# Optimization experiments

Hardware: AMD Instinct MI355X
Metric: run time of the kernel (lower is better)

The kernel has to match this reference:

```python
import jax, jax.numpy as jnp
import numpy as np

N_A, N_P, E = 50000, 50000, 600000
H, D = 8, 16
C = H * D  # hidden_channels = 128
OUT = 16
F_A, F_P = 256, 128
NEG_SLOPE = 0.2
EPS = 1e-5


def setup_inputs():
    key = jax.random.key(0)
    ks = jax.random.split(key, 16)
    return {
        'x_author': jax.random.normal(ks[0], (N_A, F_A), jnp.float32),
        'x_paper': jax.random.normal(ks[1], (N_P, F_P), jnp.float32),
        'W_a': jax.random.normal(ks[2], (F_A, C), jnp.float32) / np.sqrt(F_A).astype(np.float32),
        'b_a': jnp.zeros((C,), jnp.float32),
        'W_p': jax.random.normal(ks[3], (F_P, C), jnp.float32) / np.sqrt(F_P).astype(np.float32),
        'b_p': jnp.zeros((C,), jnp.float32),
        'att_src_ap': jax.random.normal(ks[4], (H, D), jnp.float32) * 0.1,
        'att_dst_ap': jax.random.normal(ks[5], (H, D), jnp.float32) * 0.1,
        'att_src_pp': jax.random.normal(ks[6], (H, D), jnp.float32) * 0.1,
        'att_dst_pp': jax.random.normal(ks[7], (H, D), jnp.float32) * 0.1,
        'k_W': jax.random.normal(ks[8], (C, C), jnp.float32) / np.sqrt(C).astype(np.float32),
        'k_b': jnp.zeros((C,), jnp.float32),
        'q': jax.random.normal(ks[9], (C,), jnp.float32) * 0.1,
        'norm_w': jnp.ones((C,), jnp.float32),
        'norm_b': jnp.zeros((C,), jnp.float32),
        'norm_ms': jnp.ones((C,), jnp.float32),
        'lin_W': jax.random.normal(ks[10], (C, OUT), jnp.float32) / np.sqrt(C).astype(np.float32),
        'lin_b': jnp.zeros((OUT,), jnp.float32),
        'edge_ap': jax.random.randint(ks[11], (2, E), 0, N_A),
        'edge_pp': jax.random.randint(ks[12], (2, E), 0, N_P),
    }


def _edge_type_out(h_src, h_dst, edge, a_src, a_dst, n_dst):
    # Node-level attention for one edge type (PyG HANConv per-metapath GAT).
    alpha_s = jnp.einsum('nhd,hd->nh', h_src, a_src)  # [N_src, H]
    alpha_d = jnp.einsum('nhd,hd->nh', h_dst, a_dst)  # [N_dst, H]
    src, dst = edge[0], edge[1]
    alpha = alpha_s[src] + alpha_d[dst]                       # [E, H]
    alpha = jnp.where(alpha >= 0, alpha, NEG_SLOPE * alpha)   # leaky_relu(0.2)
    m = jax.ops.segment_max(alpha, dst, num_segments=n_dst)
    e = jnp.exp(alpha - m[dst])
    denom = jax.ops.segment_sum(e, dst, num_segments=n_dst)
    attn = e / denom[dst]                                     # softmax over incoming edges
    msg = h_src[src] * attn[:, :, None]                       # [E, H, D]
    out = jax.ops.segment_sum(msg, dst, num_segments=n_dst)   # [n_dst, H, D]
    return jax.nn.relu(out.reshape(n_dst, H * D))


def reference(x_author, x_paper, W_a, b_a, W_p, b_p, att_src_ap, att_dst_ap,
              att_src_pp, att_dst_pp, k_W, k_b, q, norm_w, norm_b, norm_ms,
              lin_W, lin_b, edge_ap, edge_pp):
    # per-node-type projections -> [N, H, D]
    h_a = (x_author @ W_a + b_a).reshape(N_A, H, D)
    h_p = (x_paper @ W_p + b_p).reshape(N_P, H, D)
    # per-edge-type node-level attention + aggregation (both target 'paper')
    out_ap = _edge_type_out(h_a, h_p, edge_ap, att_src_ap, att_dst_ap, N_P)
    out_pp = _edge_type_out(h_p, h_p, edge_pp, att_src_pp, att_dst_pp, N_P)
    # semantic-level attention across the R=2 meta-paths
    outs = jnp.stack([out_ap, out_pp], axis=0)               # [R, N_P, C]
    w = jnp.tanh(outs @ k_W + k_b).mean(axis=1) @ q          # [R]
    beta = jax.nn.softmax(w)
    out = jnp.einsum('rnc,r->nc', outs, beta)                # [N_P, C]
    # GraphNorm (single graph: stats over all nodes)
    mean = out.mean(axis=0)
    o = out - mean * norm_ms
    var = (o * o).mean(axis=0)
    o = norm_w * o / jnp.sqrt(var + EPS) + norm_b
    # final classifier
    return o @ lin_W + lin_b
```

## Files before the change

kernel.cpp:

```cpp
#include <hip/hip_runtime.h>
#include <math.h>

#define NN   50000
#define EE   600000
#define CCH  128
#define HH   8
#define DD   16
#define OUTC 16
#define NEG  0.2f
#define EPSN 1e-5f
#define SLICE_DIV 12500

typedef _Float16 f16x8 __attribute__((ext_vector_type(8)));
typedef float    f32x4 __attribute__((ext_vector_type(4)));

__device__ __forceinline__ float fast_tanh(float x) {
    x = fminf(10.f, fmaxf(-10.f, x));
    float e = __expf(2.f * x);
    return (e - 1.f) / (e + 1.f);
}

__global__ __launch_bounds__(256) void prep_k(const float* __restrict__ W_a,
        const float* __restrict__ W_p, const float* __restrict__ k_W,
        const float* __restrict__ lin_W, const int* __restrict__ ea,
        const int* __restrict__ ep, _Float16* __restrict__ Wt_a,
        _Float16* __restrict__ Wt_p, _Float16* __restrict__ kWt,
        _Float16* __restrict__ linWt, int* __restrict__ counts)
{
    int b = blockIdx.x;
    if (b < 264) {
        int id = b * 256 + threadIdx.x;
        if (id < 32768) {
            int k = id >> 7, n = id & 127;
            Wt_a[n * 256 + k] = (_Float16)W_a[id];
        } else if (id < 49152) {
            int i = id - 32768; int k = i >> 7, n = i & 127;
            Wt_p[n * 128 + k] = (_Float16)W_p[i];
        } else if (id < 65536) {
            int i = id - 49152; int k = i >> 7, n = i & 127;
            kWt[n * 128 + k] = (_Float16)k_W[i];
        } else if (id < 67584) {
            int i = id - 65536; int k = i >> 4, n = i & 15;
            linWt[n * 128 + k] = (_Float16)lin_W[i];
        }
    } else {
        int bb = b - 264;
        int slice = bb & 7;
        int chunk = bb >> 3;
        int lo = slice * SLICE_DIV, hi = lo + SLICE_DIV;
        int base = chunk * 1024;
#pragma unroll
        for (int it = 0; it < 4; ++it) {
            int e = base + it * 256 + threadIdx.x;
            if (e < EE) {
                int d = ea[EE + e];
                if (d >= lo && d < hi) atomicAdd(&counts[d], 1);
            } else if (e < 2 * EE) {
                int d = NN + ep[e];
                if (d >= lo && d < hi) atomicAdd(&counts[d], 1);
            }
        }
    }
}

__global__ __launch_bounds__(256) void gemm2_k(const float* __restrict__ X_a,
        const float* __restrict__ X_p, const _Float16* __restrict__ Wt_a,
        const _Float16* __restrict__ Wt_p, const float* __restrict__ b_a,
        const float* __restrict__ b_p,
        const float* __restrict__ att_s_ap, const float* __restrict__ att_d_ap,
        const float* __restrict__ att_s_pp, const float* __restrict__ att_d_pp,
        _Float16* __restrict__ h_a, _Float16* __restrict__ h_p,
        float* __restrict__ as_ap, float* __restrict__ ad_ap,
        float* __restrict__ as_pp, float* __restrict__ ad_pp, int GBn)
{
    __shared__ _Float16 As[64][40];
    __shared__ _Float16 Bs[128][40];
    const int which = ((int)blockIdx.x >= GBn) ? 1 : 0;
    const float* X = which ? X_p : X_a;
    const _Float16* Wt = which ? Wt_p : Wt_a;
    const float* bias = which ? b_p : b_a;
    _Float16* Y = which ? h_p : h_a;
    const int K = which ? 128 : 256;
    const int t = threadIdx.x;
    const int r0 = (blockIdx.x - which * GBn) * 64;
    const int lane = t & 63;
    const int wv = t >> 6;
    const int m16 = lane & 15;
    const int kq = lane >> 4;
    f32x4 acc[8];
#pragma unroll
    for (int i = 0; i < 8; ++i) acc[i] = (f32x4){0.f, 0.f, 0.f, 0.f};

    const int ar = t >> 2;
    const int ak = (t & 3) * 8;
    const int br = t >> 1;
    const int bk = (t & 1) * 16;

    for (int kc = 0; kc < K; kc += 32) {
        int row = r0 + ar;
        f16x8 av;
        if (row < NN) {
            const float4* gp = (const float4*)&X[row * K + kc + ak];
            float4 x0 = gp[0], x1 = gp[1];
            av[0] = (_Float16)x0.x; av[1] = (_Float16)x0.y;
            av[2] = (_Float16)x0.z; av[3] = (_Float16)x0.w;
            av[4] = (_Float16)x1.x; av[5] = (_Float16)x1.y;
            av[6] = (_Float16)x1.z; av[7] = (_Float16)x1.w;
        } else {
#pragma unroll
            for (int j = 0; j < 8; ++j) av[j] = (_Float16)0.f;
        }
        *(f16x8*)&As[ar][ak] = av;
        const f16x8* wp = (const f16x8*)&Wt[br * K + kc + bk];
        *(f16x8*)&Bs[br][bk]     = wp[0];
        *(f16x8*)&Bs[br][bk + 8] = wp[1];
        __syncthreads();
        f16x8 af = *(const f16x8*)&As[wv * 16 + m16][kq * 8];
#pragma unroll
        for (int i = 0; i < 8; ++i) {
            f16x8 bf = *(const f16x8*)&Bs[i * 16 + m16][kq * 8];
            acc[i] = __builtin_amdgcn_mfma_f32_16x16x32_f16(af, bf, acc[i], 0, 0, 0);
        }
        __syncthreads();
    }
    const int rbase = r0 + wv * 16 + kq * 4;
#pragma unroll
    for (int i = 0; i < 8; ++i) {
        int col = i * 16 + m16;
        float b = bias[col];
        float hv[4];
#pragma unroll
        for (int rr = 0; rr < 4; ++rr) hv[rr] = acc[i][rr] + b;
#pragma unroll
        for (int rr = 0; rr < 4; ++rr)
            if (rbase + rr < NN) Y[(rbase + rr) * 128 + col] = (_Float16)hv[rr];
        if (which == 0) {
            float av = att_s_ap[i * 16 + m16];
            float p[4];
#pragma unroll
            for (int rr = 0; rr < 4; ++rr) p[rr] = hv[rr] * av;
#pragma unroll
            for (int x = 1; x < 16; x <<= 1)
#pragma unroll
                for (int rr = 0; rr < 4; ++rr) p[rr] += __shfl_xor(p[rr], x, 64);
            if (m16 == 0) {
#pragma unroll
                for (int rr = 0; rr < 4; ++rr)
                    if (rbase + rr < NN) as_ap[(rbase + rr) * 8 + i] = p[rr];
            }
        } else {
            float a1 = att_d_ap[i * 16 + m16];
            float a2 = att_s_pp[i * 16 + m16];
            float a3 = att_d_pp[i * 16 + m16];
            float p1[4], p2[4], p3[4];
#pragma unroll
            for (int rr = 0; rr < 4; ++rr) {
                p1[rr] = hv[rr] * a1; p2[rr] = hv[rr] * a2; p3[rr] = hv[rr] * a3;
            }
#pragma unroll
            for (int x = 1; x < 16; x <<= 1) {
#pragma unroll
                for (int rr = 0; rr < 4; ++rr) {
                    p1[rr] += __shfl_xor(p1[rr], x, 64);
                    p2[rr] += __shfl_xor(p2[rr], x, 64);
                    p3[rr] += __shfl_xor(p3[rr], x, 64);
                }
            }
            if (m16 == 0) {
#pragma unroll
                for (int rr = 0; rr < 4; ++rr) {
                    if (rbase + rr < NN) {
                        ad_ap[(rbase + rr) * 8 + i] = p1[rr];
                        as_pp[(rbase + rr) * 8 + i] = p2[rr];
                        ad_pp[(rbase + rr) * 8 + i] = p3[rr];
                    }
                }
            }
        }
    }
}

__global__ __launch_bounds__(256) void scan1_k(const int* __restrict__ counts,
        int* __restrict__ incl, int* __restrict__ bsum) {
    __shared__ int s[256];
    int t = threadIdx.x;
    int i = blockIdx.x * 256 + t;
    int v = (i < 2 * NN) ? counts[i] : 0;
    s[t] = v; __syncthreads();
    for (int off = 1; off < 256; off <<= 1) {
        int x = (t >= off) ? s[t - off] : 0;
        __syncthreads();
        s[t] += x;
        __syncthreads();
    }
    incl[i] = s[t];
    if (t == 255) bsum[blockIdx.x] = s[255];
}

__global__ __launch_bounds__(512) void scan2_k(int* __restrict__ bsum, int nb) {
    __shared__ int s[512];
    int t = threadIdx.x;
    int v = (t < nb) ? bsum[t] : 0;
    s[t] = v; __syncthreads();
    for (int off = 1; off < 512; off <<= 1) {
        int x = (t >= off) ? s[t - off] : 0;
        __syncthreads();
        s[t] += x;
        __syncthreads();
    }
    if (t < nb) bsum[t] = s[t] - v;
}

__global__ __launch_bounds__(256) void scan3_k(const int* __restrict__ incl,
        const int* __restrict__ bexcl, int* __restrict__ rp) {
    int i = blockIdx.x * 256 + threadIdx.x;
    if (i < 2 * NN) rp[i + 1] = incl[i] + bexcl[blockIdx.x];
    if (i == 0) rp[0] = 0;
}

__global__ __launch_bounds__(256) void scat_k(const int* __restrict__ ea,
        const int* __restrict__ ep, const int* __restrict__ rp,
        int* __restrict__ fill, int* __restrict__ csr)
{
    int bb = blockIdx.x;
    int slice = bb & 7;
    int chunk = bb >> 3;
    int lo = slice * SLICE_DIV, hi = lo + SLICE_DIV;
    int base = chunk * 1024;
#pragma unroll
    for (int it = 0; it < 4; ++it) {
        int e = base + it * 256 + threadIdx.x;
        if (e < EE) {
            int d = ea[EE + e];
            if (d >= lo && d < hi) {
                int pos = rp[d] + atomicAdd(&fill[d], 1);
                csr[pos] = ea[e];
            }
        } else if (e < 2 * EE) {
            int d = NN + ep[e];
            if (d >= lo && d < hi) {
                int pos = rp[d] + atomicAdd(&fill[d], 1);
                csr[pos] = ep[e - EE];
            }
        }
    }
}

__global__ __launch_bounds__(256) void agg4_k(
        const _Float16* __restrict__ h_a, const _Float16* __restrict__ h_p,
        const float* __restrict__ as_ap, const float* __restrict__ ad_ap,
        const float* __restrict__ as_pp, const float* __restrict__ ad_pp,
        const int* __restrict__ rp, const int* __restrict__ csr,
        _Float16* __restrict__ out_ap, _Float16* __restrict__ out_pp)
{
    int wave = threadIdx.x >> 6;
    int lane = threadIdx.x & 63;
    int q = lane >> 4;
    int sub = lane & 15;
    int gnode = blockIdx.x * 16 + wave * 4 + q;
    bool pp = gnode >= NN;
    int n = pp ? gnode - NN : gnode;
    const _Float16* hsrc = pp ? h_p : h_a;
    const float* as = pp ? as_pp : as_ap;
    const float* ad = pp ? ad_pp : ad_ap;
    _Float16* outb = pp ? out_pp : out_ap;
    int h = sub >> 1;
    float adv = ad[n * 8 + h];
    int p = rp[gnode], p1 = rp[gnode + 1];
    float l = 0.f;
    float acc[8] = {0.f, 0.f, 0.f, 0.f, 0.f, 0.f, 0.f, 0.f};
    for (; p + 1 < p1; p += 2) {
        int s0 = csr[p], s1 = csr[p + 1];
        float a0 = as[s0 * 8 + h] + adv;
        float a1 = as[s1 * 8 + h] + adv;
        a0 = (a0 >= 0.f) ? a0 : NEG * a0;
        a1 = (a1 >= 0.f) ? a1 : NEG * a1;
        float w0 = __expf(a0);
        float w1 = __expf(a1);
        f16x8 v0 = *(const f16x8*)&hsrc[s0 * CCH + sub * 8];
        f16x8 v1 = *(const f16x8*)&hsrc[s1 * CCH + sub * 8];
        l += w0 + w1;
#pragma unroll
        for (int i = 0; i < 8; ++i) acc[i] += w0 * (float)v0[i] + w1 * (float)v1[i];
    }
    if (p < p1) {
        int s0 = csr[p];
        float a0 = as[s0 * 8 + h] + adv;
        a0 = (a0 >= 0.f) ? a0 : NEG * a0;
        float w0 = __expf(a0);
        f16x8 v0 = *(const f16x8*)&hsrc[s0 * CCH + sub * 8];
        l += w0;
#pragma unroll
        for (int i = 0; i < 8; ++i) acc[i] += w0 * (float)v0[i];
    }
    float inv = (l > 0.f) ? 1.f / l : 0.f;
    f16x8 o;
#pragma unroll
    for (int i = 0; i < 8; ++i) o[i] = (_Float16)fmaxf(acc[i] * inv, 0.f);
    *(f16x8*)&outb[n * CCH + sub * 8] = o;
}

__global__ __launch_bounds__(256) void stats2_k(const _Float16* __restrict__ Xa,
        const _Float16* __restrict__ Xb,
        float* __restrict__ sA, float* __restrict__ sB,
        float* __restrict__ ssA, float* __restrict__ ssB, float* __restrict__ sAB)
{
    __shared__ float sbuf[640];
    int t = threadIdx.x;
    for (int i = t; i < 640; i += 256) sbuf[i] = 0.f;
    __syncthreads();
    int oct = t & 15, rs = t >> 4;
    int start = (int)blockIdx.x * 196;
    int end = start + 196; if (end > NN) end = NN;
    float sa[8] = {0,0,0,0,0,0,0,0}, sb[8] = {0,0,0,0,0,0,0,0};
    float ssa[8] = {0,0,0,0,0,0,0,0}, ssb[8] = {0,0,0,0,0,0,0,0};
    float sab[8] = {0,0,0,0,0,0,0,0};
    for (int r = start + rs; r < end; r += 16) {
        f16x8 va = *(const f16x8*)&Xa[r * 128 + oct * 8];
        f16x8 vb = *(const f16x8*)&Xb[r * 128 + oct * 8];
#pragma unroll
        for (int j = 0; j < 8; ++j) {
            float a = (float)va[j], b = (float)vb[j];
            sa[j] += a; sb[j] += b;
            ssa[j] += a * a; ssb[j] += b * b; sab[j] += a * b;
        }
    }
#pragma unroll
    for (int x = 16; x < 64; x <<= 1) {
#pragma unroll
        for (int j = 0; j < 8; ++j) {
            sa[j]  += __shfl_xor(sa[j],  x, 64);
            sb[j]  += __shfl_xor(sb[j],  x, 64);
            ssa[j] += __shfl_xor(ssa[j], x, 64);
            ssb[j] += __shfl_xor(ssb[j], x, 64);
            sab[j] += __shfl_xor(sab[j], x, 64);
        }
    }
    if ((t & 63) < 16) {
        int c0 = oct * 8;
#pragma unroll
        for (int j = 0; j < 8; ++j) {
            atomicAdd(&sbuf[c0 + j], sa[j]);
            atomicAdd(&sbuf[128 + c0 + j], sb[j]);
            atomicAdd(&sbuf[256 + c0 + j], ssa[j]);
            atomicAdd(&sbuf[384 + c0 + j], ssb[j]);
            atomicAdd(&sbuf[512 + c0 + j], sab[j]);
        }
    }
    __syncthreads();
    if (t < 128) {
        atomicAdd(&sA[t],  sbuf[t]);
        atomicAdd(&sB[t],  sbuf[128 + t]);
        atomicAdd(&ssA[t], sbuf[256 + t]);
        atomicAdd(&ssB[t], sbuf[384 + t]);
        atomicAdd(&sAB[t], sbuf[512 + t]);
    }
}

__global__ __launch_bounds__(256) void sem2_k(const _Float16* __restrict__ Xa,
        const _Float16* __restrict__ Xb, const _Float16* __restrict__ kWt,
        const float* __restrict__ kb, const float* __restrict__ q,
        float* __restrict__ wacc, int GBn)
{
    __shared__ float wred[4];
    const int b = (int)blockIdx.x;
    const int which = (b >= GBn) ? 1 : 0;
    const _Float16* Xh = which ? Xb : Xa;
    const int r0 = (b - which * GBn) * 64;
    const int t = threadIdx.x;
    const int lane = t & 63, wv = t >> 6;
    const int m16 = lane & 15, kq = lane >> 4;
    const int arow = r0 + wv * 16 + m16;
    f16x8 af[4];
    if (arow < NN) {
#pragma unroll
        for (int kc4 = 0; kc4 < 4; ++kc4)
            af[kc4] = *(const f16x8*)&Xh[arow * 128 + kc4 * 32 + kq * 8];
    } else {
#pragma unroll
        for (int kc4 = 0; kc4 < 4; ++kc4)
#pragma unroll
            for (int j = 0; j < 8; ++j) af[kc4][j] = (_Float16)0.f;
    }
    f32x4 acc[8];
#pragma unroll
    for (int i = 0; i < 8; ++i) acc[i] = (f32x4){0.f, 0.f, 0.f, 0.f};
#pragma unroll
    for (int kc4 = 0; kc4 < 4; ++kc4) {
#pragma unroll
        for (int i = 0; i < 8; ++i) {
            f16x8 bf = *(const f16x8*)&kWt[(i * 16 + m16) * 128 + kc4 * 32 + kq * 8];
            acc[i] = __builtin_amdgcn_mfma_f32_16x16x32_f16(af[kc4], bf, acc[i], 0, 0, 0);
        }
    }
    const int rbase = r0 + wv * 16 + kq * 4;
    float local = 0.f;
#pragma unroll
    for (int i = 0; i < 8; ++i) {
        float kbc = kb[i * 16 + m16], qc = q[i * 16 + m16];
#pragma unroll
        for (int rr = 0; rr < 4; ++rr)
            if (rbase + rr < NN) local += fast_tanh(acc[i][rr] + kbc) * qc;
    }
#pragma unroll
    for (int x = 1; x < 64; x <<= 1) local += __shfl_xor(local, x, 64);
    if (lane == 0) wred[wv] = local;
    __syncthreads();
    if (t == 0) {
        float s = wred[0] + wred[1] + wred[2] + wred[3];
        atomicAdd(&wacc[which * 256 + (b & 15) * 16], s);
    }
}

__global__ __launch_bounds__(256) void final2_k(
        const _Float16* __restrict__ oa, const _Float16* __restrict__ ob,
        const float* __restrict__ wacc,
        const float* __restrict__ sA, const float* __restrict__ sB,
        const float* __restrict__ ssA, const float* __restrict__ ssB,
        const float* __restrict__ sAB,
        const float* __restrict__ ms, const float* __restrict__ nw,
        const float* __restrict__ nb,
        const _Float16* __restrict__ linWt, const float* __restrict__ linb,
        float* __restrict__ out)
{
    __shared__ _Float16 As[64][136];
    __shared__ float scl[128], shf[128];
    __shared__ float bcoef[2];
    int t = threadIdx.x;
    if (t < 128) {
        float w0s = 0.f, w1s = 0.f;
#pragma unroll
        for (int i = 0; i < 16; ++i) {
            w0s += wacc[i * 16];
            w1s += wacc[256 + i * 16];
        }
        float w0 = w0s * (1.f / NN), w1 = w1s * (1.f / NN);
        float mm = fmaxf(w0, w1);
        float e0 = __expf(w0 - mm), e1 = __expf(w1 - mm);
        float b0 = e0 / (e0 + e1), b1 = e1 / (e0 + e1);
        if (t == 0) { bcoef[0] = b0; bcoef[1] = b1; }
        int c = t;
        float mean = (b0 * sA[c] + b1 * sB[c]) * (1.f / NN);
        float ex2 = (b0 * b0 * ssA[c] + 2.f * b0 * b1 * sAB[c] + b1 * b1 * ssB[c]) * (1.f / NN);
        float a = mean * ms[c];
        float var = ex2 - 2.f * a * mean + a * a;
        float sc = nw[c] * rsqrtf(var + EPSN);
        scl[c] = sc;
        shf[c] = nb[c] - a * sc;
    }
    __syncthreads();
    float b0 = bcoef[0], b1 = bcoef[1];
    int r0 = blockIdx.x * 64;
    int row = t >> 2, cp = (t & 3) * 32;
    int gr = r0 + row;
    if (gr < NN) {
#pragma unroll
        for (int i = 0; i < 4; ++i) {
            int c0 = cp + i * 8;
            f16x8 va = *(const f16x8*)&oa[gr * CCH + c0];
            f16x8 vb = *(const f16x8*)&ob[gr * CCH + c0];
            f16x8 o;
#pragma unroll
            for (int e2 = 0; e2 < 8; ++e2) {
                float v = b0 * (float)va[e2] + b1 * (float)vb[e2];
                o[e2] = (_Float16)(v * scl[c0 + e2] + shf[c0 + e2]);
            }
            *(f16x8*)&As[row][c0] = o;
        }
    } else {
        f16x8 z;
#pragma unroll
        for (int e2 = 0; e2 < 8; ++e2) z[e2] = (_Float16)0.f;
#pragma unroll
        for (int i = 0; i < 4; ++i) *(f16x8*)&As[row][cp + i * 8] = z;
    }
    __syncthreads();
    int lane = t & 63, wv = t >> 6;
    int m16 = lane & 15, kq = lane >> 4;
    f32x4 acc = (f32x4){0.f, 0.f, 0.f, 0.f};
#pragma unroll
    for (int kc = 0; kc < 128; kc += 32) {
        f16x8 af = *(const f16x8*)&As[wv * 16 + m16][kc + kq * 8];
        f16x8 bf = *(const f16x8*)&linWt[m16 * 128 + kc + kq * 8];
        acc = __builtin_amdgcn_mfma_f32_16x16x32_f16(af, bf, acc, 0, 0, 0);
    }
    float lb = linb[m16];
#pragma unroll
    for (int r = 0; r < 4; ++r) {
        int gr2 = r0 + wv * 16 + kq * 4 + r;
        if (gr2 < NN) out[gr2 * 16 + m16] = acc[r] + lb;
    }
}

extern "C" void kernel_launch(void* const* d_in, const int* in_sizes, int n_in,
                              void* d_out, int out_size, void* d_ws, size_t ws_size,
                              hipStream_t stream) {
    const float* x_a   = (const float*)d_in[0];
    const float* x_p   = (const float*)d_in[1];
    const float* W_a   = (const float*)d_in[2];
    const float* b_a   = (const float*)d_in[3];
    const float* W_p   = (const float*)d_in[4];
    const float* b_p   = (const float*)d_in[5];
    const float* att_src_ap = (const float*)d_in[6];
    const float* att_dst_ap = (const float*)d_in[7];
    const float* att_src_pp = (const float*)d_in[8];
    const float* att_dst_pp = (const float*)d_in[9];
    const float* k_W   = (const float*)d_in[10];
    const float* k_b   = (const float*)d_in[11];
    const float* q     = (const float*)d_in[12];
    const float* norm_w = (const float*)d_in[13];
    const float* norm_b = (const float*)d_in[14];
    const float* norm_ms = (const float*)d_in[15];
    const float* lin_W = (const float*)d_in[16];
    const float* lin_b = (const float*)d_in[17];
    const int* edge_ap = (const int*)d_in[18];
    const int* edge_pp = (const int*)d_in[19];
    float* out = (float*)d_out;

    char* base = (char*)d_ws;
    size_t off = 0;
    auto alloc = [&](size_t bytes) -> void* {
        void* r = base + off;
        off += (bytes + 255) & ~(size_t)255;
        return r;
    };
    _Float16* h_a    = (_Float16*)alloc((size_t)NN * CCH * 2);
    _Float16* h_p    = (_Float16*)alloc((size_t)NN * CCH * 2);
    _Float16* out_ap = (_Float16*)alloc((size_t)NN * CCH * 2);
    _Float16* out_pp = (_Float16*)alloc((size_t)NN * CCH * 2);
    float* as_ap  = (float*)alloc((size_t)NN * HH * 4);
    float* ad_ap  = (float*)alloc((size_t)NN * HH * 4);
    float* as_pp  = (float*)alloc((size_t)NN * HH * 4);
    float* ad_pp  = (float*)alloc((size_t)NN * HH * 4);
    _Float16* Wt_a = (_Float16*)alloc((size_t)128 * 256 * 2);
    _Float16* Wt_p = (_Float16*)alloc((size_t)128 * 128 * 2);
    _Float16* kWt  = (_Float16*)alloc((size_t)128 * 128 * 2);
    _Float16* linWt = (_Float16*)alloc((size_t)16 * 128 * 2);
    int* incl    = (int*)alloc((size_t)100352 * 4);
    int* bsum    = (int*)alloc(512 * 4);
    int* rp_all  = (int*)alloc((size_t)(2 * NN + 1) * 4);
    int* csr_all = (int*)alloc((size_t)2 * EE * 4);
    const size_t ZCOUNT = 100000 + 100000 + 512 + 5 * 128;
    int* zz = (int*)alloc(ZCOUNT * 4);
    int* counts = zz;
    int* fill   = zz + 100000;
    float* wacc = (float*)(zz + 200000);
    float* sA   = (float*)(zz + 200512);
    float* sB   = sA + 128;
    float* ssA  = sB + 128;
    float* ssB  = ssA + 128;
    float* sAB  = ssB + 128;

    (void)in_sizes; (void)n_in; (void)out_size; (void)ws_size;

    hipMemsetAsync(zz, 0, ZCOUNT * 4, stream);

    const int CHUNKS = (2 * EE + 1023) / 1024;
    prep_k<<<264 + CHUNKS * 8, 256, 0, stream>>>(W_a, W_p, k_W, lin_W, edge_ap, edge_pp,
                                                 Wt_a, Wt_p, kWt, linWt, counts);

    const int GB = (NN + 63) / 64;
    gemm2_k<<<2 * GB, 256, 0, stream>>>(x_a, x_p, Wt_a, Wt_p, b_a, b_p,
                                        att_src_ap, att_dst_ap, att_src_pp, att_dst_pp,
                                        h_a, h_p, as_ap, ad_ap, as_pp, ad_pp, GB);

    const int SB = 392;
    scan1_k<<<SB, 256, 0, stream>>>(counts, incl, bsum);
    scan2_k<<<1, 512, 0, stream>>>(bsum, SB);
    scan3_k<<<SB, 256, 0, stream>>>(incl, bsum, rp_all);

    scat_k<<<CHUNKS * 8, 256, 0, stream>>>(edge_ap, edge_pp, rp_all, fill, csr_all);

    agg4_k<<<2 * NN / 16, 256, 0, stream>>>(h_a, h_p, as_ap, ad_ap, as_pp, ad_pp,
                                            rp_all, csr_all, out_ap, out_pp);

    stats2_k<<<256, 256, 0, stream>>>(out_ap, out_pp, sA, sB, ssA, ssB, sAB);

    sem2_k<<<2 * GB, 256, 0, stream>>>(out_ap, out_pp, kWt, k_b, q, wacc, GB);

    final2_k<<<GB, 256, 0, stream>>>(out_ap, out_pp, wacc, sA, sB, ssA, ssB, sAB,
                                     norm_ms, norm_w, norm_b, linWt, lin_b, out);
}
```

Baseline: 403.1 us.

## Merge degree counting into GEMM launch, merge stats and semantic kernels, unroll aggregation

Moves the edge degree-count atomics out of the weight-conversion kernel and into extra blocks of the projection GEMM launch, so they run alongside the GEMM. Merges the GraphNorm statistics kernel and the semantic-attention kernel into one launch, with blocks dispatched by index. Unrolls the edge aggregation loop from 2 to 4 edges per iteration to expose more independent gathers. This saves launch gaps and improves overlap, at the cost of more register pressure in the aggregation loop and mixed block types within one launch.

```diff
diff --git a/kernel.cpp b/kernel.cpp
--- a/kernel.cpp
+++ b/kernel.cpp
@@ -10,6 +10,7 @@
 #define NEG  0.2f
 #define EPSN 1e-5f
 #define SLICE_DIV 12500
+#define CHUNKS 1172
 
 typedef _Float16 f16x8 __attribute__((ext_vector_type(8)));
 typedef float    f32x4 __attribute__((ext_vector_type(4)));
@@ -20,50 +21,29 @@
     return (e - 1.f) / (e + 1.f);
 }
 
-__global__ __launch_bounds__(256) void prep_k(const float* __restrict__ W_a,
+__global__ __launch_bounds__(256) void convw_k(const float* __restrict__ W_a,
         const float* __restrict__ W_p, const float* __restrict__ k_W,
-        const float* __restrict__ lin_W, const int* __restrict__ ea,
-        const int* __restrict__ ep, _Float16* __restrict__ Wt_a,
+        const float* __restrict__ lin_W, _Float16* __restrict__ Wt_a,
         _Float16* __restrict__ Wt_p, _Float16* __restrict__ kWt,
-        _Float16* __restrict__ linWt, int* __restrict__ counts)
+        _Float16* __restrict__ linWt)
 {
-    int b = blockIdx.x;
-    if (b < 264) {
-        int id = b * 256 + threadIdx.x;
-        if (id < 32768) {
-            int k = id >> 7, n = id & 127;
-            Wt_a[n * 256 + k] = (_Float16)W_a[id];
-        } else if (id < 49152) {
-            int i = id - 32768; int k = i >> 7, n = i & 127;
-            Wt_p[n * 128 + k] = (_Float16)W_p[i];
-        } else if (id < 65536) {
-            int i = id - 49152; int k = i >> 7, n = i & 127;
-            kWt[n * 128 + k] = (_Float16)k_W[i];
-        } else if (id < 67584) {
-            int i = id - 65536; int k = i >> 4, n = i & 15;
-            linWt[n * 128 + k] = (_Float16)lin_W[i];
-        }
-    } else {
-        int bb = b - 264;
-        int slice = bb & 7;
-        int chunk = bb >> 3;
-        int lo = slice * SLICE_DIV, hi = lo + SLICE_DIV;
-        int base = chunk * 1024;
-#pragma unroll
-        for (int it = 0; it < 4; ++it) {
-            int e = base + it * 256 + threadIdx.x;
-            if (e < EE) {
-                int d = ea[EE + e];
-                if (d >= lo && d < hi) atomicAdd(&counts[d], 1);
-            } else if (e < 2 * EE) {
-                int d = NN + ep[e];
-                if (d >= lo && d < hi) atomicAdd(&counts[d], 1);
-            }
-        }
-    }
-}
-
-__global__ __launch_bounds__(256) void gemm2_k(const float* __restrict__ X_a,
+    int id = blockIdx.x * 256 + threadIdx.x;
+    if (id < 32768) {
+        int k = id >> 7, n = id & 127;
+        Wt_a[n * 256 + k] = (_Float16)W_a[id];
+    } else if (id < 49152) {
+        int i = id - 32768; int k = i >> 7, n = i & 127;
+        Wt_p[n * 128 + k] = (_Float16)W_p[i];
+    } else if (id < 65536) {
+        int i = id - 49152; int k = i >> 7, n = i & 127;
+        kWt[n * 128 + k] = (_Float16)k_W[i];
+    } else if (id < 67584) {
+        int i = id - 65536; int k = i >> 4, n = i & 15;
+        linWt[n * 128 + k] = (_Float16)lin_W[i];
+    }
+}
+
+__global__ __launch_bounds__(256) void gemm2h_k(const float* __restrict__ X_a,
         const float* __restrict__ X_p, const _Float16* __restrict__ Wt_a,
         const _Float16* __restrict__ Wt_p, const float* __restrict__ b_a,
         const float* __restrict__ b_p,
@@ -71,17 +51,38 @@
         const float* __restrict__ att_s_pp, const float* __restrict__ att_d_pp,
         _Float16* __restrict__ h_a, _Float16* __restrict__ h_p,
         float* __restrict__ as_ap, float* __restrict__ ad_ap,
-        float* __restrict__ as_pp, float* __restrict__ ad_pp, int GBn)
+        float* __restrict__ as_pp, float* __restrict__ ad_pp,
+        const int* __restrict__ ea, const int* __restrict__ ep,
+        int* __restrict__ counts, int GBn)
 {
     __shared__ _Float16 As[64][40];
     __shared__ _Float16 Bs[128][40];
+    const int t = threadIdx.x;
+    if ((int)blockIdx.x >= 2 * GBn) {
+        int bb = (int)blockIdx.x - 2 * GBn;
+        int slice = bb & 7;
+        int chunk = bb >> 3;
+        int lo = slice * SLICE_DIV, hi = lo + SLICE_DIV;
+        int base = chunk * 1024;
+#pragma unroll
+        for (int it = 0; it < 4; ++it) {
+            int e = base + it * 256 + t;
+            if (e < EE) {
+                int d = ea[EE + e];
+                if (d >= lo && d < hi) atomicAdd(&counts[d], 1);
+            } else if (e < 2 * EE) {
+                int d = NN + ep[e];
+                if (d >= lo && d < hi) atomicAdd(&counts[d], 1);
+            }
+        }
+        return;
+    }
     const int which = ((int)blockIdx.x >= GBn) ? 1 : 0;
     const float* X = which ? X_p : X_a;
     const _Float16* Wt = which ? Wt_p : Wt_a;
     const float* bias = which ? b_p : b_a;
     _Float16* Y = which ? h_p : h_a;
     const int K = which ? 128 : 256;
-    const int t = threadIdx.x;
     const int r0 = (blockIdx.x - which * GBn) * 64;
     const int lane = t & 63;
     const int wv = t >> 6;
@@ -269,21 +270,28 @@
     int p = rp[gnode], p1 = rp[gnode + 1];
     float l = 0.f;
     float acc[8] = {0.f, 0.f, 0.f, 0.f, 0.f, 0.f, 0.f, 0.f};
-    for (; p + 1 < p1; p += 2) {
-        int s0 = csr[p], s1 = csr[p + 1];
+    for (; p + 3 < p1; p += 4) {
+        int s0 = csr[p], s1 = csr[p + 1], s2 = csr[p + 2], s3 = csr[p + 3];
         float a0 = as[s0 * 8 + h] + adv;
         float a1 = as[s1 * 8 + h] + adv;
+        float a2 = as[s2 * 8 + h] + adv;
+        float a3 = as[s3 * 8 + h] + adv;
         a0 = (a0 >= 0.f) ? a0 : NEG * a0;
         a1 = (a1 >= 0.f) ? a1 : NEG * a1;
-        float w0 = __expf(a0);
-        float w1 = __expf(a1);
+        a2 = (a2 >= 0.f) ? a2 : NEG * a2;
+        a3 = (a3 >= 0.f) ? a3 : NEG * a3;
+        float w0 = __expf(a0), w1 = __expf(a1), w2 = __expf(a2), w3 = __expf(a3);
         f16x8 v0 = *(const f16x8*)&hsrc[s0 * CCH + sub * 8];
         f16x8 v1 = *(const f16x8*)&hsrc[s1 * CCH + sub * 8];
-        l += w0 + w1;
-#pragma unroll
-        for (int i = 0; i < 8; ++i) acc[i] += w0 * (float)v0[i] + w1 * (float)v1[i];
-    }
-    if (p < p1) {
+        f16x8 v2 = *(const f16x8*)&hsrc[s2 * CCH + sub * 8];
+        f16x8 v3 = *(const f16x8*)&hsrc[s3 * CCH + sub * 8];
+        l += (w0 + w1) + (w2 + w3);
+#pragma unroll
+        for (int i = 0; i < 8; ++i)
+            acc[i] += (w0 * (float)v0[i] + w1 * (float)v1[i])
+                    + (w2 * (float)v2[i] + w3 * (float)v3[i]);
+    }
+    for (; p < p1; ++p) {
         int s0 = csr[p];
         float a0 = as[s0 * 8 + h] + adv;
         a0 = (a0 >= 0.f) ? a0 : NEG * a0;
@@ -300,115 +308,111 @@
     *(f16x8*)&outb[n * CCH + sub * 8] = o;
 }
 
-__global__ __launch_bounds__(256) void stats2_k(const _Float16* __restrict__ Xa,
-        const _Float16* __restrict__ Xb,
-        float* __restrict__ sA, float* __restrict__ sB,
-        float* __restrict__ ssA, float* __restrict__ ssB, float* __restrict__ sAB)
+__global__ __launch_bounds__(256) void semstats2_k(const _Float16* __restrict__ Xa,
+        const _Float16* __restrict__ Xb, const _Float16* __restrict__ kWt,
+        const float* __restrict__ kb, const float* __restrict__ q,
+        float* __restrict__ wacc, float* __restrict__ sA, float* __restrict__ sB,
+        float* __restrict__ ssA, float* __restrict__ ssB, float* __restrict__ sAB,
+        int GBn)
 {
     __shared__ float sbuf[640];
-    int t = threadIdx.x;
-    for (int i = t; i < 640; i += 256) sbuf[i] = 0.f;
-    __syncthreads();
-    int oct = t & 15, rs = t >> 4;
-    int start = (int)blockIdx.x * 196;
-    int end = start + 196; if (end > NN) end = NN;
-    float sa[8] = {0,0,0,0,0,0,0,0}, sb[8] = {0,0,0,0,0,0,0,0};
-    float ssa[8] = {0,0,0,0,0,0,0,0}, ssb[8] = {0,0,0,0,0,0,0,0};
-    float sab[8] = {0,0,0,0,0,0,0,0};
-    for (int r = start + rs; r < end; r += 16) {
-        f16x8 va = *(const f16x8*)&Xa[r * 128 + oct * 8];
-        f16x8 vb = *(const f16x8*)&Xb[r * 128 + oct * 8];
-#pragma unroll
-        for (int j = 0; j < 8; ++j) {
-            float a = (float)va[j], b = (float)vb[j];
-            sa[j] += a; sb[j] += b;
-            ssa[j] += a * a; ssb[j] += b * b; sab[j] += a * b;
-        }
-    }
-#pragma unroll
-    for (int x = 16; x < 64; x <<= 1) {
-#pragma unroll
-        for (int j = 0; j < 8; ++j) {
-            sa[j]  += __shfl_xor(sa[j],  x, 64);
-            sb[j]  += __shfl_xor(sb[j],  x, 64);
-            ssa[j] += __shfl_xor(ssa[j], x, 64);
-            ssb[j] += __shfl_xor(ssb[j], x, 64);
-            sab[j] += __shfl_xor(sab[j], x, 64);
-        }
-    }
-    if ((t & 63) < 16) {
-        int c0 = oct * 8;
-#pragma unroll
-        for (int j = 0; j < 8; ++j) {
-            atomicAdd(&sbuf[c0 + j], sa[j]);
-            atomicAdd(&sbuf[128 + c0 + j], sb[j]);
-            atomicAdd(&sbuf[256 + c0 + j], ssa[j]);
-            atomicAdd(&sbuf[384 + c0 + j], ssb[j]);
-            atomicAdd(&sbuf[512 + c0 + j], sab[j]);
-        }
-    }
-    __syncthreads();
-    if (t < 128) {
-        atomicAdd(&sA[t],  sbuf[t]);
-        atomicAdd(&sB[t],  sbuf[128 + t]);
-        atomicAdd(&ssA[t], sbuf[256 + t]);
-        atomicAdd(&ssB[t], sbuf[384 + t]);
-        atomicAdd(&sAB[t], sbuf[512 + t]);
-    }
-}
-
-__global__ __launch_bounds__(256) void sem2_k(const _Float16* __restrict__ Xa,
-        const _Float16* __restrict__ Xb, const _Float16* __restrict__ kWt,
-        const float* __restrict__ kb, const float* __restrict__ q,
-        float* __restrict__ wacc, int GBn)
-{
-    __shared__ float wred[4];
-    const int b = (int)blockIdx.x;
-    const int which = (b >= GBn) ? 1 : 0;
-    const _Float16* Xh = which ? Xb : Xa;
-    const int r0 = (b - which * GBn) * 64;
     const int t = threadIdx.x;
-    const int lane = t & 63, wv = t >> 6;
-    const int m16 = lane & 15, kq = lane >> 4;
-    const int arow = r0 + wv * 16 + m16;
-    f16x8 af[4];
-    if (arow < NN) {
-#pragma unroll
-        for (int kc4 = 0; kc4 < 4; ++kc4)
-            af[kc4] = *(const f16x8*)&Xh[arow * 128 + kc4 * 32 + kq * 8];
+    if ((int)blockIdx.x < 256) {
+        for (int i = t; i < 640; i += 256) sbuf[i] = 0.f;
+        __syncthreads();
+        int oct = t & 15, rs = t >> 4;
+        int start = (int)blockIdx.x * 196;
+        int end = start + 196; if (end > NN) end = NN;
+        float sa[8] = {0,0,0,0,0,0,0,0}, sb[8] = {0,0,0,0,0,0,0,0};
+        float ssa[8] = {0,0,0,0,0,0,0,0}, ssb[8] = {0,0,0,0,0,0,0,0};
+        float sab[8] = {0,0,0,0,0,0,0,0};
+        for (int r = start + rs; r < end; r += 16) {
+            f16x8 va = *(const f16x8*)&Xa[r * 128 + oct * 8];
+            f16x8 vb = *(const f16x8*)&Xb[r * 128 + oct * 8];
+#pragma unroll
+            for (int j = 0; j < 8; ++j) {
+                float a = (float)va[j], b = (float)vb[j];
+                sa[j] += a; sb[j] += b;
+                ssa[j] += a * a; ssb[j] += b * b; sab[j] += a * b;
+            }
+        }
+#pragma unroll
+        for (int x = 16; x < 64; x <<= 1) {
+#pragma unroll
+            for (int j = 0; j < 8; ++j) {
+                sa[j]  += __shfl_xor(sa[j],  x, 64);
+                sb[j]  += __shfl_xor(sb[j],  x, 64);
+                ssa[j] += __shfl_xor(ssa[j], x, 64);
+                ssb[j] += __shfl_xor(ssb[j], x, 64);
+                sab[j] += __shfl_xor(sab[j], x, 64);
+            }
+        }
+        if ((t & 63) < 16) {
+            int c0 = oct * 8;
+#pragma unroll
+            for (int j = 0; j < 8; ++j) {
+                atomicAdd(&sbuf[c0 + j], sa[j]);
+                atomicAdd(&sbuf[128 + c0 + j], sb[j]);
+                atomicAdd(&sbuf[256 + c0 + j], ssa[j]);
+                atomicAdd(&sbuf[384 + c0 + j], ssb[j]);
+                atomicAdd(&sbuf[512 + c0 + j], sab[j]);
+            }
+        }
+        __syncthreads();
+        if (t < 128) {
+            atomicAdd(&sA[t],  sbuf[t]);
+            atomicAdd(&sB[t],  sbuf[128 + t]);
+            atomicAdd(&ssA[t], sbuf[256 + t]);
+            atomicAdd(&ssB[t], sbuf[384 + t]);
+            atomicAdd(&sAB[t], sbuf[512 + t]);
+        }
     } else {
-#pragma unroll
-        for (int kc4 = 0; kc4 < 4; ++kc4)
-#pragma unroll
-            for (int j = 0; j < 8; ++j) af[kc4][j] = (_Float16)0.f;
-    }
-    f32x4 acc[8];
-#pragma unroll
-    for (int i = 0; i < 8; ++i) acc[i] = (f32x4){0.f, 0.f, 0.f, 0.f};
-#pragma unroll
-    for (int kc4 = 0; kc4 < 4; ++kc4) {
+        const int b = (int)blockIdx.x - 256;
+        const int which = (b >= GBn) ? 1 : 0;
+        const _Float16* Xh = which ? Xb : Xa;
+        const int r0 = (b - which * GBn) * 64;
+        const int lane = t & 63, wv = t >> 6;
+        const int m16 = lane & 15, kq = lane >> 4;
+        const int arow = r0 + wv * 16 + m16;
+        f16x8 af[4];
+        if (arow < NN) {
+#pragma unroll
+            for (int kc4 = 0; kc4 < 4; ++kc4)
+                af[kc4] = *(const f16x8*)&Xh[arow * 128 + kc4 * 32 + kq * 8];
+        } else {
+#pragma unroll
+            for (int kc4 = 0; kc4 < 4; ++kc4)
+#pragma unroll
+                for (int j = 0; j < 8; ++j) af[kc4][j] = (_Float16)0.f;
+        }
+        f32x4 acc[8];
+#pragma unroll
+        for (int i = 0; i < 8; ++i) acc[i] = (f32x4){0.f, 0.f, 0.f, 0.f};
+#pragma unroll
+        for (int kc4 = 0; kc4 < 4; ++kc4) {
+#pragma unroll
+            for (int i = 0; i < 8; ++i) {
+                f16x8 bf = *(const f16x8*)&kWt[(i * 16 + m16) * 128 + kc4 * 32 + kq * 8];
+                acc[i] = __builtin_amdgcn_mfma_f32_16x16x32_f16(af[kc4], bf, acc[i], 0, 0, 0);
+            }
+        }
+        const int rbase = r0 + wv * 16 + kq * 4;
+        float local = 0.f;
 #pragma unroll
         for (int i = 0; i < 8; ++i) {
-            f16x8 bf = *(const f16x8*)&kWt[(i * 16 + m16) * 128 + kc4 * 32 + kq * 8];
-            acc[i] = __builtin_amdgcn_mfma_f32_16x16x32_f16(af[kc4], bf, acc[i], 0, 0, 0);
-        }
-    }
-    const int rbase = r0 + wv * 16 + kq * 4;
-    float local = 0.f;
-#pragma unroll
-    for (int i = 0; i < 8; ++i) {
-        float kbc = kb[i * 16 + m16], qc = q[i * 16 + m16];
-#pragma unroll
-        for (int rr = 0; rr < 4; ++rr)
-            if (rbase + rr < NN) local += fast_tanh(acc[i][rr] + kbc) * qc;
-    }
-#pragma unroll
-    for (int x = 1; x < 64; x <<= 1) local += __shfl_xor(local, x, 64);
-    if (lane == 0) wred[wv] = local;
-    __syncthreads();
-    if (t == 0) {
-        float s = wred[0] + wred[1] + wred[2] + wred[3];
-        atomicAdd(&wacc[which * 256 + (b & 15) * 16], s);
+            float kbc = kb[i * 16 + m16], qc = q[i * 16 + m16];
+#pragma unroll
+            for (int rr = 0; rr < 4; ++rr)
+                if (rbase + rr < NN) local += fast_tanh(acc[i][rr] + kbc) * qc;
+        }
+#pragma unroll
+        for (int x = 1; x < 64; x <<= 1) local += __shfl_xor(local, x, 64);
+        if (lane == 0) sbuf[wv] = local;
+        __syncthreads();
+        if (t == 0) {
+            float s = sbuf[0] + sbuf[1] + sbuf[2] + sbuf[3];
+            atomicAdd(&wacc[which * 256 + (b & 15) * 16], s);
+        }
     }
 }
 
@@ -555,14 +559,14 @@
 
     hipMemsetAsync(zz, 0, ZCOUNT * 4, stream);
 
-    const int CHUNKS = (2 * EE + 1023) / 1024;
-    prep_k<<<264 + CHUNKS * 8, 256, 0, stream>>>(W_a, W_p, k_W, lin_W, edge_ap, edge_pp,
-                                                 Wt_a, Wt_p, kWt, linWt, counts);
+    convw_k<<<264, 256, 0, stream>>>(W_a, W_p, k_W, lin_W, Wt_a, Wt_p, kWt, linWt);
 
     const int GB = (NN + 63) / 64;
-    gemm2_k<<<2 * GB, 256, 0, stream>>>(x_a, x_p, Wt_a, Wt_p, b_a, b_p,
-                                        att_src_ap, att_dst_ap, att_src_pp, att_dst_pp,
-                                        h_a, h_p, as_ap, ad_ap, as_pp, ad_pp, GB);
+    gemm2h_k<<<2 * GB + CHUNKS * 8, 256, 0, stream>>>(
+        x_a, x_p, Wt_a, Wt_p, b_a, b_p,
+        att_src_ap, att_dst_ap, att_src_pp, att_dst_pp,
+        h_a, h_p, as_ap, ad_ap, as_pp, ad_pp,
+        edge_ap, edge_pp, counts, GB);
 
     const int SB = 392;
     scan1_k<<<SB, 256, 0, stream>>>(counts, incl, bsum);
@@ -574,9 +578,8 @@
     agg4_k<<<2 * NN / 16, 256, 0, stream>>>(h_a, h_p, as_ap, ad_ap, as_pp, ad_pp,
                                             rp_all, csr_all, out_ap, out_pp);
 
-    stats2_k<<<256, 256, 0, stream>>>(out_ap, out_pp, sA, sB, ssA, ssB, sAB);
-
-    sem2_k<<<2 * GB, 256, 0, stream>>>(out_ap, out_pp, kWt, k_b, q, wacc, GB);
+    semstats2_k<<<256 + 2 * GB, 256, 0, stream>>>(out_ap, out_pp, kWt, k_b, q, wacc,
+                                                  sA, sB, ssA, ssB, sAB, GB);
 
     final2_k<<<GB, 256, 0, stream>>>(out_ap, out_pp, wacc, sA, sB, ssA, ssB, sAB,
                                      norm_ms, norm_w, norm_b, linWt, lin_b, out);
```

Measured after the change: 376.7 us. -6.5%, faster.
